# Kernel optimization log

Measured on AMD Instinct MI355X. Metric: run time of the kernel, lower is better.

## Reference

```python
import jax, jax.numpy as jnp
import numpy as np
from jax import lax

H = 50  # hidden size hard-coded in DocSenModel

def setup_inputs() -> dict:
    key = jax.random.key(0)
    ks = jax.random.split(key, 16)
    V, E, S, W, O = 100000, 300, 64, 64, 5
    def n(k, shape, scale=0.05):
        return jax.random.normal(k, shape, jnp.float32) * scale
    return {
        "doc": jax.random.randint(ks[0], (S, W), 0, V),      # [S sentences, W words]
        "emb": n(ks[1], (V, E), 1.0),                        # embedding table
        "W_word": n(ks[2], (H, E)), "b_word": jnp.zeros(H, jnp.float32),
        "conv_w1": n(ks[3], (H, H, 1)), "conv_b1": jnp.zeros(H, jnp.float32),
        "conv_w2": n(ks[4], (H, H, 2)), "conv_b2": jnp.zeros(H, jnp.float32),
        "conv_w3": n(ks[5], (H, H, 3)), "conv_b3": jnp.zeros(H, jnp.float32),
        # forward GNN gates: input_layer (i), forget_gate (f), input_gate (g)
        "Wf_i": n(ks[6], (H, 2 * H)), "bf_i": jnp.zeros(H, jnp.float32),
        "Wf_f": n(ks[7], (H, 2 * H)), "bf_f": jnp.zeros(H, jnp.float32),
        "Wf_g": n(ks[8], (H, 2 * H)), "bf_g": jnp.zeros(H, jnp.float32),
        # backward GNN gates
        "Wb_i": n(ks[9], (H, 2 * H)), "bb_i": jnp.zeros(H, jnp.float32),
        "Wb_f": n(ks[10], (H, 2 * H)), "bb_f": jnp.zeros(H, jnp.float32),
        "Wb_g": n(ks[11], (H, 2 * H)), "bb_g": jnp.zeros(H, jnp.float32),
        "W_out": n(ks[12], (O, 2 * H)), "b_out": jnp.zeros(O, jnp.float32),
    }


def _gnn_step(Wi, bi, Wf, bf, Wg, bg):
    # h_t = tanh(sigmoid(Wi[x,h]) * tanh(Wg[x,h]) + sigmoid(Wf[x,h]) * h)
    def step(h, x):
        comp = jnp.concatenate([x, h])
        i_t = jax.nn.sigmoid(Wi @ comp + bi)
        f_t = jax.nn.sigmoid(Wf @ comp + bf)
        g_t = jnp.tanh(Wg @ comp + bg)
        h_t = jnp.tanh(i_t * g_t + f_t * h)
        return h_t, h_t
    return step


def reference(doc, emb, W_word, b_word,
              conv_w1, conv_b1, conv_w2, conv_b2, conv_w3, conv_b3,
              Wf_i, bf_i, Wf_f, bf_f, Wf_g, bf_g,
              Wb_i, bb_i, Wb_f, bb_f, Wb_g, bb_g,
              W_out, b_out):
    # --- per-word embedding + linear projection, batched over all sentences ---
    x = emb[doc]                                        # [S, W, E]
    words = jnp.einsum('swe,he->swh', x, W_word) + b_word  # [S, W, H]
    c_in = words.transpose(0, 2, 1)                     # [S, H, W]  (NCW)

    # --- sentence convolution: conv_k -> avg-pool over full length -> tanh, mean over k ---
    def conv_rep(w, b):
        y = lax.conv_general_dilated(c_in, w, (1,), 'VALID',
                                     dimension_numbers=('NCW', 'OIW', 'NCW'))
        y = y + b[None, :, None]
        return jnp.tanh(y.mean(axis=2))                 # [S, H]

    reps = (conv_rep(conv_w1, conv_b1)
            + conv_rep(conv_w2, conv_b2)
            + conv_rep(conv_w3, conv_b3)) / 3.0          # [S, H]  (mean over 3 kernels)

    # --- bidirectional gated recurrent GNN chain over sentence reps ---
    h0 = jnp.zeros(H, reps.dtype)
    _, hs_f = lax.scan(_gnn_step(Wf_i, bf_i, Wf_f, bf_f, Wf_g, bf_g), h0, reps)
    _, hs_b = lax.scan(_gnn_step(Wb_i, bb_i, Wb_f, bb_f, Wb_g, bb_g), h0, reps[::-1])
    hs_b = hs_b[::-1]                                   # align backward states to sentence order

    combined = jnp.concatenate([hs_f, hs_b], axis=1)    # [S, 2H]
    gnn_out = combined.mean(axis=0)                     # [2H]
    return jax.nn.softmax(W_out @ gnn_out + b_out)      # [output_size]
```

## Files before the change

kernel.cpp:

```cpp
#include <hip/hip_runtime.h>
#include <math.h>

#define NS 64
#define NW 64
#define NE 300
#define NH 50
#define NO 5


typedef __fp16 half2v __attribute__((ext_vector_type(2)));

__device__ __forceinline__ float fdot2(half2v a, half2v b, float c) {
  return __builtin_amdgcn_fdot2(a, b, c, false);
}
__device__ __forceinline__ float fast_tanh(float x) {
  x = fminf(15.f, fmaxf(-15.f, x));
  const float e = __expf(2.f * x);
  return 1.f - 2.f * __builtin_amdgcn_rcpf(e + 1.f);
}
__device__ __forceinline__ float fast_sigmoid(float x) {
  return __builtin_amdgcn_rcpf(1.f + __expf(-x));
}


__global__ __launch_bounds__(512) void k_reps(
    const int* __restrict__ doc, const float* __restrict__ emb,
    const float* __restrict__ Wword, const float* __restrict__ bword,
    const float* __restrict__ w1, const float* __restrict__ b1,
    const float* __restrict__ w2, const float* __restrict__ b2,
    const float* __restrict__ w3, const float* __restrict__ b3,
    const float* __restrict__ Wfi, const float* __restrict__ bfi,
    const float* __restrict__ Wff, const float* __restrict__ bff,
    const float* __restrict__ Wfg, const float* __restrict__ bfg,
    const float* __restrict__ Wbi, const float* __restrict__ bbi,
    const float* __restrict__ Wbf, const float* __restrict__ bbf,
    const float* __restrict__ Wbg, const float* __restrict__ bbg,
    float* __restrict__ Xg, unsigned int* __restrict__ pw)
{
  __shared__ int   idxs[NW];
  __shared__ float sv[5][304];
  __shared__ float ph1[304];
  __shared__ float dots[5][NH];
  __shared__ float reps_s[NH];

  const int s = blockIdx.x, tid = threadIdx.x;

  if (s == NS) {
    for (int idx = tid; idx < 7500; idx += 512) {
      const int j  = idx % 50;
      const int c  = (idx / 50) % 25;
      const int dg = idx / 1250;
      const float* Wp;
      switch (dg) {
        case 0: Wp = Wfi; break;
        case 1: Wp = Wff; break;
        case 2: Wp = Wfg; break;
        case 3: Wp = Wbi; break;
        case 4: Wp = Wbf; break;
        default: Wp = Wbg; break;
      }
      const int base = j * 100 + 50 + 2 * c;
      const half2v v = __builtin_amdgcn_cvt_pkrtz(Wp[base], Wp[base + 1]);
      pw[idx] = __builtin_bit_cast(unsigned int, v);
    }
    return;
  }

  if (tid < NW) idxs[tid] = doc[s * NW + tid];
  __syncthreads();

  const int p = tid >> 8, et = tid & 255;
  for (int e = et; e < NE; e += 256) {
    float acc = 0.f;
    const int w0 = p * 32;
#pragma unroll 16
    for (int w = w0; w < w0 + 32; ++w)
      acc += emb[(size_t)idxs[w] * NE + e];
    if (p == 0) sv[0][e] = acc; else ph1[e] = acc;
    if (p == 0) {
      sv[1][e] = emb[(size_t)idxs[0]  * NE + e];
      sv[2][e] = emb[(size_t)idxs[1]  * NE + e];
    } else {
      sv[3][e] = emb[(size_t)idxs[62] * NE + e];
      sv[4][e] = emb[(size_t)idxs[63] * NE + e];
    }
  }
  __syncthreads();
  if (tid < NE) sv[0][tid] += ph1[tid];
  __syncthreads();

  if (tid < 5 * NH) {
    const int fam = tid / NH, i = tid % NH;
    const float4* v4 = (const float4*)&sv[fam][0];
    const float4* w4 = (const float4*)(Wword + (size_t)i * NE);
    float a0 = 0.f, a1 = 0.f;
#pragma unroll
    for (int c = 0; c < NE / 4; ++c) {
      const float4 v = v4[c], w = w4[c];
      a0 += v.x * w.x + v.y * w.y;
      a1 += v.z * w.z + v.w * w.w;
    }
    dots[fam][i] = a0 + a1;
  }
  __syncthreads();

  if (tid < 8 * NH) {
    const int o = tid >> 3, part = tid & 7;
    float m1 = 0.f, m2 = 0.f, m3 = 0.f;
    for (int i = part; i < NH; i += 8) {
      const float bw    = bword[i];
      const float total = dots[0][i] + 64.f * bw;
      const float e0  = dots[1][i] + bw;
      const float e1  = dots[2][i] + bw;
      const float e62 = dots[3][i] + bw;
      const float e63 = dots[4][i] + bw;
      m1 += w1[o * NH + i] * total;
      m2 += w2[(o * NH + i) * 2 + 0] * (total - e63)
          + w2[(o * NH + i) * 2 + 1] * (total - e0);
      m3 += w3[(o * NH + i) * 3 + 0] * (total - e62 - e63)
          + w3[(o * NH + i) * 3 + 1] * (total - e0 - e63)
          + w3[(o * NH + i) * 3 + 2] * (total - e0 - e1);
    }
#pragma unroll
    for (int m = 1; m < 8; m <<= 1) {
      m1 += __shfl_xor(m1, m);
      m2 += __shfl_xor(m2, m);
      m3 += __shfl_xor(m3, m);
    }
    if (part == 0) {
      m1 = b1[o] + m1 * (1.f / 64.f);
      m2 = b2[o] + m2 * (1.f / 63.f);
      m3 = b3[o] + m3 * (1.f / 62.f);
      reps_s[o] = (fast_tanh(m1) + fast_tanh(m2) + fast_tanh(m3)) * (1.f / 3.f);
    }
  }
  __syncthreads();

  if (tid < 6 * NH) {
    const int dg = tid / NH, j = tid % NH;
    const float* Wp; const float* bp;
    switch (dg) {
      case 0: Wp = Wfi; bp = bfi; break;
      case 1: Wp = Wff; bp = bff; break;
      case 2: Wp = Wfg; bp = bfg; break;
      case 3: Wp = Wbi; bp = bbi; break;
      case 4: Wp = Wbf; bp = bbf; break;
      default: Wp = Wbg; bp = bbg; break;
    }
    float acc = bp[j];
    for (int k = 0; k < NH; ++k) acc += Wp[j * 100 + k] * reps_s[k];
    const int dir = dg / 3, gate = dg % 3;
    Xg[((dir * NS + s) * 3 + gate) * NH + j] = acc;
  }
}

struct X3 { float i, f, g; };

__global__ __launch_bounds__(128, 1) void k_scan(
    const float* __restrict__ Xg, const unsigned int* __restrict__ pw,
    const float* __restrict__ Wout, const float* __restrict__ bout,
    float* __restrict__ out)
{
  __shared__ float gsum_sh[2 * NH];

  const int tid = threadIdx.x;
  const int d   = tid >> 6;
  const int lane = tid & 63;
  const int j   = (lane < NH) ? lane : 0;

  half2v wi2[25], wf2[25], wg2[25];
#pragma unroll
  for (int c = 0; c < 25; ++c) {
    wi2[c] = __builtin_bit_cast(half2v, pw[((d * 3 + 0) * 25 + c) * 50 + j]);
    wf2[c] = __builtin_bit_cast(half2v, pw[((d * 3 + 1) * 25 + c) * 50 + j]);
    wg2[c] = __builtin_bit_cast(half2v, pw[((d * 3 + 2) * 25 + c) * 50 + j]);
  }

  const float* Xd = Xg + d * NS * 3 * NH;

  auto ldx = [&](int t) -> X3 {
    const int tt = d ? (NS - 1 - t) : t;
    X3 r;
    r.i = Xd[tt * 150 + j];
    r.f = Xd[tt * 150 + 50 + j];
    r.g = Xd[tt * 150 + 100 + j];
    return r;
  };

  float hj = 0.f, hs = 0.f;

  auto dostep = [&](X3 x) {
    float ai0 = x.i, af0 = x.f, ag0 = x.g;
    float ai1 = 0.f, af1 = 0.f, ag1 = 0.f;
    const float hpart = __builtin_bit_cast(float,
        __builtin_amdgcn_ds_swizzle(__builtin_bit_cast(int, hj), 0x041F));
    const half2v hpk = __builtin_amdgcn_cvt_pkrtz(hj, hpart);
    const int packed = __builtin_bit_cast(int, hpk);
#pragma unroll
    for (int c = 0; c < 25; ++c) {
      const half2v hk2 = __builtin_bit_cast(half2v,
          __builtin_amdgcn_readlane(packed, 2 * c));
      if (c & 1) {
        ai1 = fdot2(wi2[c], hk2, ai1);
        af1 = fdot2(wf2[c], hk2, af1);
        ag1 = fdot2(wg2[c], hk2, ag1);
      } else {
        ai0 = fdot2(wi2[c], hk2, ai0);
        af0 = fdot2(wf2[c], hk2, af0);
        ag0 = fdot2(wg2[c], hk2, ag0);
      }
    }
    const float it = fast_sigmoid(ai0 + ai1);
    const float ft = fast_sigmoid(af0 + af1);
    const float gt = fast_tanh(ag0 + ag1);
    hj = fast_tanh(it * gt + ft * hj);
    hs += hj;
  };

  X3 p0 = ldx(0), p1 = ldx(1), p2 = ldx(2), p3 = ldx(3);

#pragma unroll 1
  for (int k = 0; k < NS / 4; ++k) {
    const int n = 4 * k;
    const int q0 = (n + 4 < NS) ? n + 4 : NS - 1;
    const int q1 = (n + 5 < NS) ? n + 5 : NS - 1;
    const int q2 = (n + 6 < NS) ? n + 6 : NS - 1;
    const int q3 = (n + 7 < NS) ? n + 7 : NS - 1;
    X3 c0 = p0; p0 = ldx(q0); dostep(c0);
    X3 c1 = p1; p1 = ldx(q1); dostep(c1);
    X3 c2 = p2; p2 = ldx(q2); dostep(c2);
    X3 c3 = p3; p3 = ldx(q3); dostep(c3);
  }

  if (lane < NH) gsum_sh[d * NH + lane] = hs * (1.f / 64.f);
  __syncthreads();

  if (d == 0) {
    float lg = 0.f;
    if (lane < NO) {
      float acc = bout[lane];
      for (int k = 0; k < 2 * NH; ++k) acc += Wout[lane * 2 * NH + k] * gsum_sh[k];
      lg = acc;
    }
    const float l0 = __shfl(lg, 0), l1 = __shfl(lg, 1), l2 = __shfl(lg, 2),
                l3 = __shfl(lg, 3), l4 = __shfl(lg, 4);
    if (lane == 0) {
      const float m = fmaxf(fmaxf(fmaxf(l0, l1), fmaxf(l2, l3)), l4);
      const float e0 = __expf(l0 - m), e1 = __expf(l1 - m), e2 = __expf(l2 - m),
                  e3 = __expf(l3 - m), e4 = __expf(l4 - m);
      const float se = e0 + e1 + e2 + e3 + e4;
      out[0] = e0 / se; out[1] = e1 / se; out[2] = e2 / se;
      out[3] = e3 / se; out[4] = e4 / se;
    }
  }
}

extern "C" void kernel_launch(void* const* d_in, const int* in_sizes, int n_in,
                              void* d_out, int out_size, void* d_ws, size_t ws_size,
                              hipStream_t stream) {
  const int*   doc   = (const int*)  d_in[0];
  const float* emb   = (const float*)d_in[1];
  const float* Wword = (const float*)d_in[2];
  const float* bword = (const float*)d_in[3];
  const float* w1    = (const float*)d_in[4];
  const float* b1    = (const float*)d_in[5];
  const float* w2    = (const float*)d_in[6];
  const float* b2    = (const float*)d_in[7];
  const float* w3    = (const float*)d_in[8];
  const float* b3    = (const float*)d_in[9];
  const float* Wfi   = (const float*)d_in[10];
  const float* bfi   = (const float*)d_in[11];
  const float* Wff   = (const float*)d_in[12];
  const float* bff   = (const float*)d_in[13];
  const float* Wfg   = (const float*)d_in[14];
  const float* bfg   = (const float*)d_in[15];
  const float* Wbi   = (const float*)d_in[16];
  const float* bbi   = (const float*)d_in[17];
  const float* Wbf   = (const float*)d_in[18];
  const float* bbf   = (const float*)d_in[19];
  const float* Wbg   = (const float*)d_in[20];
  const float* bbg   = (const float*)d_in[21];
  const float* Wout  = (const float*)d_in[22];
  const float* bout  = (const float*)d_in[23];

  float* Xg = (float*)d_ws + 64;
  unsigned int* pw = (unsigned int*)((float*)d_ws + 64 + 19200);

  k_reps<<<dim3(NS + 1), dim3(512), 0, stream>>>(
      doc, emb, Wword, bword, w1, b1, w2, b2, w3, b3,
      Wfi, bfi, Wff, bff, Wfg, bfg, Wbi, bbi, Wbf, bbf, Wbg, bbg,
      Xg, pw);

  k_scan<<<dim3(1), dim3(128), 0, stream>>>(
      Xg, pw, Wout, bout, (float*)d_out);
}
```

Before: 37.93 us.

## Split GNN scan gates across six wavefronts with LDS exchange per step

The recurrent scan kernel grows from 2 wavefronts (one per direction, each computing all three gates) to 6 wavefronts, one per direction-gate pair. Each wave does a third of the fp16 dot products per step, and gate activations are exchanged through double-buffered shared memory with a block barrier every timestep. The ds_swizzle is replaced by a DPP quad permute, and the packed weight layout now uses a 64-stride. This shortens each step's serial dot-product chain but adds a __syncthreads and LDS round trip to every one of the 64 sequential steps.

```diff
diff --git a/kernel.cpp b/kernel.cpp
--- a/kernel.cpp
+++ b/kernel.cpp
@@ -46,10 +46,11 @@
   const int s = blockIdx.x, tid = threadIdx.x;
 
   if (s == NS) {
-    for (int idx = tid; idx < 7500; idx += 512) {
+#pragma unroll 8
+    for (int idx = tid; idx < 6 * 25 * 50; idx += 512) {
       const int j  = idx % 50;
       const int c  = (idx / 50) % 25;
-      const int dg = idx / 1250;
+      const int dg = idx / (25 * 50);
       const float* Wp;
       switch (dg) {
         case 0: Wp = Wfi; break;
@@ -61,7 +62,7 @@
       }
       const int base = j * 100 + 50 + 2 * c;
       const half2v v = __builtin_amdgcn_cvt_pkrtz(Wp[base], Wp[base + 1]);
-      pw[idx] = __builtin_bit_cast(unsigned int, v);
+      pw[(dg * 25 + c) * 64 + j] = __builtin_bit_cast(unsigned int, v);
     }
     return;
   }
@@ -154,88 +155,74 @@
   }
 }
 
-struct X3 { float i, f, g; };
-
-__global__ __launch_bounds__(128, 1) void k_scan(
+__global__ __launch_bounds__(384, 1) void k_scan(
     const float* __restrict__ Xg, const unsigned int* __restrict__ pw,
     const float* __restrict__ Wout, const float* __restrict__ bout,
     float* __restrict__ out)
 {
+  __shared__ float gate_sh[2][2][3][64];
   __shared__ float gsum_sh[2 * NH];
 
-  const int tid = threadIdx.x;
-  const int d   = tid >> 6;
-  const int lane = tid & 63;
-  const int j   = (lane < NH) ? lane : 0;
-
-  half2v wi2[25], wf2[25], wg2[25];
-#pragma unroll
-  for (int c = 0; c < 25; ++c) {
-    wi2[c] = __builtin_bit_cast(half2v, pw[((d * 3 + 0) * 25 + c) * 50 + j]);
-    wf2[c] = __builtin_bit_cast(half2v, pw[((d * 3 + 1) * 25 + c) * 50 + j]);
-    wg2[c] = __builtin_bit_cast(half2v, pw[((d * 3 + 2) * 25 + c) * 50 + j]);
-  }
-
-  const float* Xd = Xg + d * NS * 3 * NH;
-
-  auto ldx = [&](int t) -> X3 {
+  const int tid  = threadIdx.x;
+  const int wid  = tid >> 6, lane = tid & 63;
+  const int d    = wid / 3, g = wid % 3;
+  const int j    = (lane < NH) ? lane : 0;
+  const int dg   = d * 3 + g;
+
+  unsigned int wu[25];
+#pragma unroll
+  for (int c = 0; c < 25; ++c) wu[c] = pw[(dg * 25 + c) * 64 + j];
+
+  const float* Xd = Xg + d * NS * 3 * NH + g * NH + j;
+  auto ldx = [&](int t) -> float {
     const int tt = d ? (NS - 1 - t) : t;
-    X3 r;
-    r.i = Xd[tt * 150 + j];
-    r.f = Xd[tt * 150 + 50 + j];
-    r.g = Xd[tt * 150 + 100 + j];
-    return r;
+    return Xd[tt * 150];
   };
 
   float hj = 0.f, hs = 0.f;
-
-  auto dostep = [&](X3 x) {
-    float ai0 = x.i, af0 = x.f, ag0 = x.g;
-    float ai1 = 0.f, af1 = 0.f, ag1 = 0.f;
-    const float hpart = __builtin_bit_cast(float,
-        __builtin_amdgcn_ds_swizzle(__builtin_bit_cast(int, hj), 0x041F));
-    const half2v hpk = __builtin_amdgcn_cvt_pkrtz(hj, hpart);
+  float p0 = ldx(0), p1 = ldx(1), p2 = ldx(2), p3 = ldx(3);
+
+#pragma unroll 1
+  for (int n = 0; n < NS; ++n) {
+    const float x = p0;
+    p0 = p1; p1 = p2; p2 = p3;
+    const int q = (n + 4 < NS) ? n + 4 : NS - 1;
+    p3 = ldx(q);
+
+    const int hpi = __builtin_amdgcn_update_dpp(
+        0, __builtin_bit_cast(int, hj), 0xB1, 0xF, 0xF, true);
+    const half2v hpk = __builtin_amdgcn_cvt_pkrtz(
+        hj, __builtin_bit_cast(float, hpi));
     const int packed = __builtin_bit_cast(int, hpk);
+
+    float a0 = x, a1 = 0.f;
 #pragma unroll
     for (int c = 0; c < 25; ++c) {
       const half2v hk2 = __builtin_bit_cast(half2v,
           __builtin_amdgcn_readlane(packed, 2 * c));
-      if (c & 1) {
-        ai1 = fdot2(wi2[c], hk2, ai1);
-        af1 = fdot2(wf2[c], hk2, af1);
-        ag1 = fdot2(wg2[c], hk2, ag1);
-      } else {
-        ai0 = fdot2(wi2[c], hk2, ai0);
-        af0 = fdot2(wf2[c], hk2, af0);
-        ag0 = fdot2(wg2[c], hk2, ag0);
-      }
-    }
-    const float it = fast_sigmoid(ai0 + ai1);
-    const float ft = fast_sigmoid(af0 + af1);
-    const float gt = fast_tanh(ag0 + ag1);
-    hj = fast_tanh(it * gt + ft * hj);
+      const half2v wv = __builtin_bit_cast(half2v, wu[c]);
+      if (c & 1) a1 = fdot2(wv, hk2, a1);
+      else       a0 = fdot2(wv, hk2, a0);
+    }
+    const float a = a0 + a1;
+
+    const float act = (g == 2) ? fast_tanh(a) : fast_sigmoid(a);
+    const int par = n & 1;
+    if (lane < NH) gate_sh[par][d][g][lane] = act;
+
+    __syncthreads();
+
+    const float iv = gate_sh[par][d][0][j];
+    const float fv = gate_sh[par][d][1][j];
+    const float gv = gate_sh[par][d][2][j];
+    hj = fast_tanh(iv * gv + fv * hj);
     hs += hj;
-  };
-
-  X3 p0 = ldx(0), p1 = ldx(1), p2 = ldx(2), p3 = ldx(3);
-
-#pragma unroll 1
-  for (int k = 0; k < NS / 4; ++k) {
-    const int n = 4 * k;
-    const int q0 = (n + 4 < NS) ? n + 4 : NS - 1;
-    const int q1 = (n + 5 < NS) ? n + 5 : NS - 1;
-    const int q2 = (n + 6 < NS) ? n + 6 : NS - 1;
-    const int q3 = (n + 7 < NS) ? n + 7 : NS - 1;
-    X3 c0 = p0; p0 = ldx(q0); dostep(c0);
-    X3 c1 = p1; p1 = ldx(q1); dostep(c1);
-    X3 c2 = p2; p2 = ldx(q2); dostep(c2);
-    X3 c3 = p3; p3 = ldx(q3); dostep(c3);
-  }
-
-  if (lane < NH) gsum_sh[d * NH + lane] = hs * (1.f / 64.f);
-  __syncthreads();
-
-  if (d == 0) {
+  }
+
+  if (g == 0 && lane < NH) gsum_sh[d * NH + lane] = hs * (1.f / 64.f);
+  __syncthreads();
+
+  if (wid == 0) {
     float lg = 0.f;
     if (lane < NO) {
       float acc = bout[lane];
@@ -291,6 +278,6 @@
       Wfi, bfi, Wff, bff, Wfg, bfg, Wbi, bbi, Wbf, bbf, Wbg, bbg,
       Xg, pw);
 
-  k_scan<<<dim3(1), dim3(128), 0, stream>>>(
+  k_scan<<<dim3(1), dim3(384), 0, stream>>>(
       Xg, pw, Wout, bout, (float*)d_out);
 }
```

Result: slower. 45.76 us (+20.6%).

## Fuse reps and scan kernels with per-sentence flags so scan overlaps production

Applied to the files above, without the earlier changes.

Merges the two kernels into one launch. Blocks 0..63 compute the per-sentence gate inputs and publish a release flag each; block 64 packs the recurrent weights into LDS and runs the bidirectional scan, spinning on each sentence's flag before loading its inputs. This removes the second kernel launch and lets the scan start while sentences are still being produced. In exchange it adds a memset launch to clear the flags, relies on all 65 blocks being co-resident to avoid deadlock, and adds spin-wait latency inside the serial chain.

```diff
diff --git a/kernel.cpp b/kernel.cpp
--- a/kernel.cpp
+++ b/kernel.cpp
@@ -23,7 +23,9 @@
 }
 
 
-__global__ __launch_bounds__(512) void k_reps(
+struct X3 { float i, f, g; };
+
+__global__ __launch_bounds__(512, 1) void k_fused(
     const int* __restrict__ doc, const float* __restrict__ emb,
     const float* __restrict__ Wword, const float* __restrict__ bword,
     const float* __restrict__ w1, const float* __restrict__ b1,
@@ -35,207 +37,226 @@
     const float* __restrict__ Wbi, const float* __restrict__ bbi,
     const float* __restrict__ Wbf, const float* __restrict__ bbf,
     const float* __restrict__ Wbg, const float* __restrict__ bbg,
-    float* __restrict__ Xg, unsigned int* __restrict__ pw)
+    const float* __restrict__ Wout, const float* __restrict__ bout,
+    float* __restrict__ ws, float* __restrict__ out)
 {
+  int*   flags = (int*)ws;
+  float* XgG   = ws + 64;
+
   __shared__ int   idxs[NW];
   __shared__ float sv[5][304];
   __shared__ float ph1[304];
   __shared__ float dots[5][NH];
   __shared__ float reps_s[NH];
-
-  const int s = blockIdx.x, tid = threadIdx.x;
-
-  if (s == NS) {
-    for (int idx = tid; idx < 7500; idx += 512) {
-      const int j  = idx % 50;
-      const int c  = (idx / 50) % 25;
-      const int dg = idx / 1250;
-      const float* Wp;
+  __shared__ unsigned int pwl[6 * 50 * 27];
+  __shared__ float gsum_sh[2 * NH];
+
+  const int b = blockIdx.x, tid = threadIdx.x;
+
+  if (b < NS) {
+    const int s = b;
+    if (tid < NW) idxs[tid] = doc[s * NW + tid];
+    __syncthreads();
+
+    const int p = tid >> 8, et = tid & 255;
+    for (int e = et; e < NE; e += 256) {
+      float acc = 0.f;
+      const int w0 = p * 32;
+#pragma unroll 16
+      for (int w = w0; w < w0 + 32; ++w)
+        acc += emb[(size_t)idxs[w] * NE + e];
+      if (p == 0) sv[0][e] = acc; else ph1[e] = acc;
+      if (p == 0) {
+        sv[1][e] = emb[(size_t)idxs[0]  * NE + e];
+        sv[2][e] = emb[(size_t)idxs[1]  * NE + e];
+      } else {
+        sv[3][e] = emb[(size_t)idxs[62] * NE + e];
+        sv[4][e] = emb[(size_t)idxs[63] * NE + e];
+      }
+    }
+    __syncthreads();
+    if (tid < NE) sv[0][tid] += ph1[tid];
+    __syncthreads();
+
+    if (tid < 5 * NH) {
+      const int fam = tid / NH, i = tid % NH;
+      const float4* v4 = (const float4*)&sv[fam][0];
+      const float4* w4 = (const float4*)(Wword + (size_t)i * NE);
+      float a0 = 0.f, a1 = 0.f;
+#pragma unroll
+      for (int c = 0; c < NE / 4; ++c) {
+        const float4 v = v4[c], w = w4[c];
+        a0 += v.x * w.x + v.y * w.y;
+        a1 += v.z * w.z + v.w * w.w;
+      }
+      dots[fam][i] = a0 + a1;
+    }
+    __syncthreads();
+
+    if (tid < 8 * NH) {
+      const int o = tid >> 3, part = tid & 7;
+      float m1 = 0.f, m2 = 0.f, m3 = 0.f;
+      for (int i = part; i < NH; i += 8) {
+        const float bw    = bword[i];
+        const float total = dots[0][i] + 64.f * bw;
+        const float e0  = dots[1][i] + bw;
+        const float e1  = dots[2][i] + bw;
+        const float e62 = dots[3][i] + bw;
+        const float e63 = dots[4][i] + bw;
+        m1 += w1[o * NH + i] * total;
+        m2 += w2[(o * NH + i) * 2 + 0] * (total - e63)
+            + w2[(o * NH + i) * 2 + 1] * (total - e0);
+        m3 += w3[(o * NH + i) * 3 + 0] * (total - e62 - e63)
+            + w3[(o * NH + i) * 3 + 1] * (total - e0 - e63)
+            + w3[(o * NH + i) * 3 + 2] * (total - e0 - e1);
+      }
+#pragma unroll
+      for (int m = 1; m < 8; m <<= 1) {
+        m1 += __shfl_xor(m1, m);
+        m2 += __shfl_xor(m2, m);
+        m3 += __shfl_xor(m3, m);
+      }
+      if (part == 0) {
+        m1 = b1[o] + m1 * (1.f / 64.f);
+        m2 = b2[o] + m2 * (1.f / 63.f);
+        m3 = b3[o] + m3 * (1.f / 62.f);
+        reps_s[o] = (fast_tanh(m1) + fast_tanh(m2) + fast_tanh(m3)) * (1.f / 3.f);
+      }
+    }
+    __syncthreads();
+
+    if (tid < 6 * NH) {
+      const int dg = tid / NH, j = tid % NH;
+      const float* Wp; const float* bp;
       switch (dg) {
-        case 0: Wp = Wfi; break;
-        case 1: Wp = Wff; break;
-        case 2: Wp = Wfg; break;
-        case 3: Wp = Wbi; break;
-        case 4: Wp = Wbf; break;
-        default: Wp = Wbg; break;
-      }
-      const int base = j * 100 + 50 + 2 * c;
-      const half2v v = __builtin_amdgcn_cvt_pkrtz(Wp[base], Wp[base + 1]);
-      pw[idx] = __builtin_bit_cast(unsigned int, v);
+        case 0: Wp = Wfi; bp = bfi; break;
+        case 1: Wp = Wff; bp = bff; break;
+        case 2: Wp = Wfg; bp = bfg; break;
+        case 3: Wp = Wbi; bp = bbi; break;
+        case 4: Wp = Wbf; bp = bbf; break;
+        default: Wp = Wbg; bp = bbg; break;
+      }
+      float acc = bp[j];
+      for (int k = 0; k < NH; ++k) acc += Wp[j * 100 + k] * reps_s[k];
+      const int dir = dg / 3, gate = dg % 3;
+      XgG[((dir * NS + s) * 3 + gate) * NH + j] = acc;
+    }
+    __syncthreads();
+
+    if (tid == 0) {
+      __threadfence();
+      __hip_atomic_store(flags + s, 1, __ATOMIC_RELEASE,
+                         __HIP_MEMORY_SCOPE_AGENT);
     }
     return;
   }
 
-  if (tid < NW) idxs[tid] = doc[s * NW + tid];
-  __syncthreads();
-
-  const int p = tid >> 8, et = tid & 255;
-  for (int e = et; e < NE; e += 256) {
-    float acc = 0.f;
-    const int w0 = p * 32;
-#pragma unroll 16
-    for (int w = w0; w < w0 + 32; ++w)
-      acc += emb[(size_t)idxs[w] * NE + e];
-    if (p == 0) sv[0][e] = acc; else ph1[e] = acc;
-    if (p == 0) {
-      sv[1][e] = emb[(size_t)idxs[0]  * NE + e];
-      sv[2][e] = emb[(size_t)idxs[1]  * NE + e];
-    } else {
-      sv[3][e] = emb[(size_t)idxs[62] * NE + e];
-      sv[4][e] = emb[(size_t)idxs[63] * NE + e];
-    }
+#pragma unroll 4
+  for (int idx = tid; idx < 6 * 50 * 25; idx += 512) {
+    const int c  = idx % 25;
+    const int j  = (idx / 25) % 50;
+    const int dg = idx / (25 * 50);
+    const float* Wp;
+    switch (dg) {
+      case 0: Wp = Wfi; break;
+      case 1: Wp = Wff; break;
+      case 2: Wp = Wfg; break;
+      case 3: Wp = Wbi; break;
+      case 4: Wp = Wbf; break;
+      default: Wp = Wbg; break;
+    }
+    const int base = j * 100 + 50 + 2 * c;
+    const half2v v = __builtin_amdgcn_cvt_pkrtz(Wp[base], Wp[base + 1]);
+    pwl[(dg * 50 + j) * 27 + c] = __builtin_bit_cast(unsigned int, v);
   }
   __syncthreads();
-  if (tid < NE) sv[0][tid] += ph1[tid];
-  __syncthreads();
-
-  if (tid < 5 * NH) {
-    const int fam = tid / NH, i = tid % NH;
-    const float4* v4 = (const float4*)&sv[fam][0];
-    const float4* w4 = (const float4*)(Wword + (size_t)i * NE);
-    float a0 = 0.f, a1 = 0.f;
+
+  if (tid < 128) {
+    const int d   = tid >> 6;
+    const int lane = tid & 63;
+    const int j   = (lane < NH) ? lane : 0;
+
+    half2v wi2[25], wf2[25], wg2[25];
 #pragma unroll
-    for (int c = 0; c < NE / 4; ++c) {
-      const float4 v = v4[c], w = w4[c];
-      a0 += v.x * w.x + v.y * w.y;
-      a1 += v.z * w.z + v.w * w.w;
-    }
-    dots[fam][i] = a0 + a1;
+    for (int c = 0; c < 25; ++c) {
+      wi2[c] = __builtin_bit_cast(half2v, pwl[((d * 3 + 0) * 50 + j) * 27 + c]);
+      wf2[c] = __builtin_bit_cast(half2v, pwl[((d * 3 + 1) * 50 + j) * 27 + c]);
+      wg2[c] = __builtin_bit_cast(half2v, pwl[((d * 3 + 2) * 50 + j) * 27 + c]);
+    }
+
+    const float* Xd = XgG + d * NS * 3 * NH;
+
+    auto waitrdy = [&](int t) {
+      const int tt = d ? (NS - 1 - t) : t;
+      while (__hip_atomic_load(flags + tt, __ATOMIC_ACQUIRE,
+                               __HIP_MEMORY_SCOPE_AGENT) == 0)
+        __builtin_amdgcn_s_sleep(1);
+    };
+    auto ldx = [&](int t) -> X3 {
+      const int tt = d ? (NS - 1 - t) : t;
+      X3 r;
+      r.i = Xd[tt * 150 + j];
+      r.f = Xd[tt * 150 + 50 + j];
+      r.g = Xd[tt * 150 + 100 + j];
+      return r;
+    };
+
+    float hj = 0.f, hs = 0.f;
+
+    auto dostep = [&](X3 x) {
+      float ai0 = x.i, af0 = x.f, ag0 = x.g;
+      float ai1 = 0.f, af1 = 0.f, ag1 = 0.f;
+      const float hpart = __builtin_bit_cast(float,
+          __builtin_amdgcn_ds_swizzle(__builtin_bit_cast(int, hj), 0x041F));
+      const half2v hpk = __builtin_amdgcn_cvt_pkrtz(hj, hpart);
+      const int packed = __builtin_bit_cast(int, hpk);
+#pragma unroll
+      for (int c = 0; c < 25; ++c) {
+        const half2v hk2 = __builtin_bit_cast(half2v,
+            __builtin_amdgcn_readlane(packed, 2 * c));
+        if (c & 1) {
+          ai1 = fdot2(wi2[c], hk2, ai1);
+          af1 = fdot2(wf2[c], hk2, af1);
+          ag1 = fdot2(wg2[c], hk2, ag1);
+        } else {
+          ai0 = fdot2(wi2[c], hk2, ai0);
+          af0 = fdot2(wf2[c], hk2, af0);
+          ag0 = fdot2(wg2[c], hk2, ag0);
+        }
+      }
+      const float it = fast_sigmoid(ai0 + ai1);
+      const float ft = fast_sigmoid(af0 + af1);
+      const float gt = fast_tanh(ag0 + ag1);
+      hj = fast_tanh(it * gt + ft * hj);
+      hs += hj;
+    };
+
+    waitrdy(0); waitrdy(1); waitrdy(2); waitrdy(3);
+    X3 p0 = ldx(0), p1 = ldx(1), p2 = ldx(2), p3 = ldx(3);
+
+#pragma unroll 1
+    for (int k = 0; k < NS / 4; ++k) {
+      const int n = 4 * k;
+      X3 c0 = p0; p0 = p1; p1 = p2; p2 = p3;
+      dostep(c0);
+      if (n + 4 < NS) { waitrdy(n + 4); p3 = ldx(n + 4); }
+      X3 c1 = p0; p0 = p1; p1 = p2; p2 = p3;
+      dostep(c1);
+      if (n + 5 < NS) { waitrdy(n + 5); p3 = ldx(n + 5); }
+      X3 c2 = p0; p0 = p1; p1 = p2; p2 = p3;
+      dostep(c2);
+      if (n + 6 < NS) { waitrdy(n + 6); p3 = ldx(n + 6); }
+      X3 c3 = p0; p0 = p1; p1 = p2; p2 = p3;
+      dostep(c3);
+      if (n + 7 < NS) { waitrdy(n + 7); p3 = ldx(n + 7); }
+    }
+
+    if (lane < NH) gsum_sh[d * NH + lane] = hs * (1.f / 64.f);
   }
   __syncthreads();
 
-  if (tid < 8 * NH) {
-    const int o = tid >> 3, part = tid & 7;
-    float m1 = 0.f, m2 = 0.f, m3 = 0.f;
-    for (int i = part; i < NH; i += 8) {
-      const float bw    = bword[i];
-      const float total = dots[0][i] + 64.f * bw;
-      const float e0  = dots[1][i] + bw;
-      const float e1  = dots[2][i] + bw;
-      const float e62 = dots[3][i] + bw;
-      const float e63 = dots[4][i] + bw;
-      m1 += w1[o * NH + i] * total;
-      m2 += w2[(o * NH + i) * 2 + 0] * (total - e63)
-          + w2[(o * NH + i) * 2 + 1] * (total - e0);
-      m3 += w3[(o * NH + i) * 3 + 0] * (total - e62 - e63)
-          + w3[(o * NH + i) * 3 + 1] * (total - e0 - e63)
-          + w3[(o * NH + i) * 3 + 2] * (total - e0 - e1);
-    }
-#pragma unroll
-    for (int m = 1; m < 8; m <<= 1) {
-      m1 += __shfl_xor(m1, m);
-      m2 += __shfl_xor(m2, m);
-      m3 += __shfl_xor(m3, m);
-    }
-    if (part == 0) {
-      m1 = b1[o] + m1 * (1.f / 64.f);
-      m2 = b2[o] + m2 * (1.f / 63.f);
-      m3 = b3[o] + m3 * (1.f / 62.f);
-      reps_s[o] = (fast_tanh(m1) + fast_tanh(m2) + fast_tanh(m3)) * (1.f / 3.f);
-    }
-  }
-  __syncthreads();
-
-  if (tid < 6 * NH) {
-    const int dg = tid / NH, j = tid % NH;
-    const float* Wp; const float* bp;
-    switch (dg) {
-      case 0: Wp = Wfi; bp = bfi; break;
-      case 1: Wp = Wff; bp = bff; break;
-      case 2: Wp = Wfg; bp = bfg; break;
-      case 3: Wp = Wbi; bp = bbi; break;
-      case 4: Wp = Wbf; bp = bbf; break;
-      default: Wp = Wbg; bp = bbg; break;
-    }
-    float acc = bp[j];
-    for (int k = 0; k < NH; ++k) acc += Wp[j * 100 + k] * reps_s[k];
-    const int dir = dg / 3, gate = dg % 3;
-    Xg[((dir * NS + s) * 3 + gate) * NH + j] = acc;
-  }
-}
-
-struct X3 { float i, f, g; };
-
-__global__ __launch_bounds__(128, 1) void k_scan(
-    const float* __restrict__ Xg, const unsigned int* __restrict__ pw,
-    const float* __restrict__ Wout, const float* __restrict__ bout,
-    float* __restrict__ out)
-{
-  __shared__ float gsum_sh[2 * NH];
-
-  const int tid = threadIdx.x;
-  const int d   = tid >> 6;
-  const int lane = tid & 63;
-  const int j   = (lane < NH) ? lane : 0;
-
-  half2v wi2[25], wf2[25], wg2[25];
-#pragma unroll
-  for (int c = 0; c < 25; ++c) {
-    wi2[c] = __builtin_bit_cast(half2v, pw[((d * 3 + 0) * 25 + c) * 50 + j]);
-    wf2[c] = __builtin_bit_cast(half2v, pw[((d * 3 + 1) * 25 + c) * 50 + j]);
-    wg2[c] = __builtin_bit_cast(half2v, pw[((d * 3 + 2) * 25 + c) * 50 + j]);
-  }
-
-  const float* Xd = Xg + d * NS * 3 * NH;
-
-  auto ldx = [&](int t) -> X3 {
-    const int tt = d ? (NS - 1 - t) : t;
-    X3 r;
-    r.i = Xd[tt * 150 + j];
-    r.f = Xd[tt * 150 + 50 + j];
-    r.g = Xd[tt * 150 + 100 + j];
-    return r;
-  };
-
-  float hj = 0.f, hs = 0.f;
-
-  auto dostep = [&](X3 x) {
-    float ai0 = x.i, af0 = x.f, ag0 = x.g;
-    float ai1 = 0.f, af1 = 0.f, ag1 = 0.f;
-    const float hpart = __builtin_bit_cast(float,
-        __builtin_amdgcn_ds_swizzle(__builtin_bit_cast(int, hj), 0x041F));
-    const half2v hpk = __builtin_amdgcn_cvt_pkrtz(hj, hpart);
-    const int packed = __builtin_bit_cast(int, hpk);
-#pragma unroll
-    for (int c = 0; c < 25; ++c) {
-      const half2v hk2 = __builtin_bit_cast(half2v,
-          __builtin_amdgcn_readlane(packed, 2 * c));
-      if (c & 1) {
-        ai1 = fdot2(wi2[c], hk2, ai1);
-        af1 = fdot2(wf2[c], hk2, af1);
-        ag1 = fdot2(wg2[c], hk2, ag1);
-      } else {
-        ai0 = fdot2(wi2[c], hk2, ai0);
-        af0 = fdot2(wf2[c], hk2, af0);
-        ag0 = fdot2(wg2[c], hk2, ag0);
-      }
-    }
-    const float it = fast_sigmoid(ai0 + ai1);
-    const float ft = fast_sigmoid(af0 + af1);
-    const float gt = fast_tanh(ag0 + ag1);
-    hj = fast_tanh(it * gt + ft * hj);
-    hs += hj;
-  };
-
-  X3 p0 = ldx(0), p1 = ldx(1), p2 = ldx(2), p3 = ldx(3);
-
-#pragma unroll 1
-  for (int k = 0; k < NS / 4; ++k) {
-    const int n = 4 * k;
-    const int q0 = (n + 4 < NS) ? n + 4 : NS - 1;
-    const int q1 = (n + 5 < NS) ? n + 5 : NS - 1;
-    const int q2 = (n + 6 < NS) ? n + 6 : NS - 1;
-    const int q3 = (n + 7 < NS) ? n + 7 : NS - 1;
-    X3 c0 = p0; p0 = ldx(q0); dostep(c0);
-    X3 c1 = p1; p1 = ldx(q1); dostep(c1);
-    X3 c2 = p2; p2 = ldx(q2); dostep(c2);
-    X3 c3 = p3; p3 = ldx(q3); dostep(c3);
-  }
-
-  if (lane < NH) gsum_sh[d * NH + lane] = hs * (1.f / 64.f);
-  __syncthreads();
-
-  if (d == 0) {
+  if (tid < 64) {
+    const int lane = tid;
     float lg = 0.f;
     if (lane < NO) {
       float acc = bout[lane];
@@ -283,14 +304,10 @@
   const float* Wout  = (const float*)d_in[22];
   const float* bout  = (const float*)d_in[23];
 
-  float* Xg = (float*)d_ws + 64;
-  unsigned int* pw = (unsigned int*)((float*)d_ws + 64 + 19200);
-
-  k_reps<<<dim3(NS + 1), dim3(512), 0, stream>>>(
+  hipMemsetAsync(d_ws, 0, 256, stream);
+
+  k_fused<<<dim3(NS + 1), dim3(512), 0, stream>>>(
       doc, emb, Wword, bword, w1, b1, w2, b2, w3, b3,
       Wfi, bfi, Wff, bff, Wfg, bfg, Wbi, bbi, Wbf, bbf, Wbg, bbg,
-      Xg, pw);
-
-  k_scan<<<dim3(1), dim3(128), 0, stream>>>(
-      Xg, pw, Wout, bout, (float*)d_out);
-}
+      Wout, bout, (float*)d_ws, (float*)d_out);
+}
```

After: 60.54 us. 1.6x slower.
